# Performance work log

Hardware: AMD Instinct MI355X
Metric: run time of the kernel (lower is better)

## Reference

```python
import jax, jax.numpy as jnp
import numpy as np

NUM_HEADS = 16
INPUT_DIM = 1024  # == dim == qkv_scale


def setup_inputs() -> dict:
    key = jax.random.key(0)
    k1, k2, k3 = jax.random.split(key, 3)
    x = jax.random.normal(k1, (4, 2048, INPUT_DIM), dtype=jnp.float32)
    # torch Linear(input_dim, 3*dim): y = x @ W.T + b; we store W pre-transposed as [in, out]
    W_qkv = jax.random.normal(k2, (INPUT_DIM, 3 * INPUT_DIM), dtype=jnp.float32) * (INPUT_DIM ** -0.5)
    b_qkv = jax.random.normal(k3, (3 * INPUT_DIM,), dtype=jnp.float32) * 0.01
    return {"x": x, "W_qkv": W_qkv, "b_qkv": b_qkv}


def reference(x, W_qkv, b_qkv):
    b, n, _ = x.shape
    h = NUM_HEADS
    d = INPUT_DIM // h
    scale = INPUT_DIM ** 0.5  # qkv_scale**0.5, MULTIPLIED (no softmax, no division)

    qkv = x @ W_qkv + b_qkv                      # [b, n, 3*dim]
    # rearrange 'b n (h d k) -> k b h n d': last axis splits (h, d, 3), k fastest
    qkv = qkv.reshape(b, n, h, d, 3)
    q = jnp.transpose(qkv[..., 0], (0, 2, 1, 3))  # [b, h, n, d]
    k_ = jnp.transpose(qkv[..., 1], (0, 2, 1, 3))
    v = jnp.transpose(qkv[..., 2], (0, 2, 1, 3))

    attn = jnp.einsum('bhid,bhjd->bhij', q, k_) * scale  # [b, h, n, n]
    out = jnp.einsum('bhij,bhjd->bhid', attn, v)         # [b, h, n, d]
    return out
```

## Files before the change

kernel.cpp:

```cpp
#include <hip/hip_runtime.h>
#include <stdint.h>

#define DEV __device__ __forceinline__

typedef float f32x4 __attribute__((ext_vector_type(4)));
typedef __bf16 bf16x8 __attribute__((ext_vector_type(8)));
typedef short short8 __attribute__((ext_vector_type(8)));
typedef short short4v __attribute__((ext_vector_type(4)));

DEV unsigned short f2bf(float f) {
    union { float f; unsigned u; } c; c.f = f;
    unsigned u = c.u;
    u += 0x7fffu + ((u >> 16) & 1u);
    return (unsigned short)(u >> 16);
}

DEV void async_ld16(const void* g, void* l) {
    __builtin_amdgcn_global_load_lds(
        (const __attribute__((address_space(1))) unsigned int*)g,
        (__attribute__((address_space(3))) unsigned int*)l, 16, 0, 0);
}

DEV f32x4 mfma16(bf16x8 a, bf16x8 b, f32x4 c) {
    return __builtin_amdgcn_mfma_f32_16x16x32_bf16(a, b, c, 0, 0, 0);
}

__global__ __launch_bounds__(256) void k_prep(const float* __restrict__ x,
                                              const float* __restrict__ W,
                                              unsigned short* __restrict__ xb,
                                              unsigned short* __restrict__ Wt) {
    __shared__ float T[64][65];
    int blk = blockIdx.x;
    if (blk < 4096) {
        int t = blk * 256 + threadIdx.x;
        const float4* xp = (const float4*)x;
        float4 a = xp[t * 2], b = xp[t * 2 + 1];
        short8 o;
        o[0] = (short)f2bf(a.x); o[1] = (short)f2bf(a.y);
        o[2] = (short)f2bf(a.z); o[3] = (short)f2bf(a.w);
        o[4] = (short)f2bf(b.x); o[5] = (short)f2bf(b.y);
        o[6] = (short)f2bf(b.z); o[7] = (short)f2bf(b.w);
        *(short8*)(xb + t * 8) = o;
    } else {
        int bx = blk - 4096;
        int n0 = (bx % 48) * 64, k0 = (bx / 48) * 64;
        int t = threadIdx.x;
        int r = t >> 4, c4 = (t & 15) * 4;
        for (int i = 0; i < 4; i++) {
            int row = r + i * 16;
            float4 v = *(const float4*)(W + (k0 + row) * 3072 + n0 + c4);
            T[row][c4] = v.x; T[row][c4 + 1] = v.y; T[row][c4 + 2] = v.z; T[row][c4 + 3] = v.w;
        }
        __syncthreads();
        for (int i = 0; i < 4; i++) {
            int nrow = r + i * 16;
            short4v o;
            o[0] = (short)f2bf(T[c4 + 0][nrow]);
            o[1] = (short)f2bf(T[c4 + 1][nrow]);
            o[2] = (short)f2bf(T[c4 + 2][nrow]);
            o[3] = (short)f2bf(T[c4 + 3][nrow]);
            *(short4v*)(Wt + (n0 + nrow) * 1024 + k0 + c4) = o;
        }
    }
}

__global__ __launch_bounds__(256, 2) void k_qkv(const unsigned short* __restrict__ xb,
                                                const unsigned short* __restrict__ Wt,
                                                const float* __restrict__ bias,
                                                unsigned short* __restrict__ Q,
                                                unsigned short* __restrict__ K,
                                                unsigned short* __restrict__ V) {
    __shared__ __align__(16) unsigned short As[128 * 64];
    __shared__ __align__(16) unsigned short Bs[128 * 64];
    const int m0 = blockIdx.y * 128, n0 = blockIdx.x * 128;
    const int wave = threadIdx.x >> 6, lane = threadIdx.x & 63;
    const int wm = (wave & 1) * 64, wn = (wave >> 1) * 64;
    f32x4 acc[4][4] = {};
    const int slr = wave * 32 + (lane >> 3);
    const int scs = lane & 7;

    for (int kt = 0; kt < 16; kt++) {
        __syncthreads();
        for (int i = 0; i < 4; i++) {
            int lr = slr + i * 8;
            int c = scs ^ (lr & 7);
            async_ld16(xb + (m0 + lr) * 1024 + kt * 64 + c * 8,
                       (void*)(As + (wave * 32 + i * 8) * 64));
            async_ld16(Wt + (n0 + lr) * 1024 + kt * 64 + c * 8,
                       (void*)(Bs + (wave * 32 + i * 8) * 64));
        }
        __syncthreads();
        for (int ks = 0; ks < 2; ks++) {
            bf16x8 af[4], bfr[4];
            int c0 = ks * 4 + (lane >> 4);
            for (int tm = 0; tm < 4; tm++) {
                int row = wm + tm * 16 + (lane & 15);
                af[tm] = *(const bf16x8*)(As + row * 64 + (c0 ^ (row & 7)) * 8);
            }
            for (int tn = 0; tn < 4; tn++) {
                int row = wn + tn * 16 + (lane & 15);
                bfr[tn] = *(const bf16x8*)(Bs + row * 64 + (c0 ^ (row & 7)) * 8);
            }
            for (int tm = 0; tm < 4; tm++)
                for (int tn = 0; tn < 4; tn++)
                    acc[tm][tn] = mfma16(af[tm], bfr[tn], acc[tm][tn]);
        }
    }

    const int batch = m0 >> 11;
    for (int tn = 0; tn < 4; tn++) {
        int col = n0 + wn + tn * 16 + (lane & 15);
        int h = col / 192;
        int rem = col - h * 192;
        int d = rem / 3;
        int which = rem - d * 3;
        float bv = bias[col];
        int bh = batch * 16 + h;
        unsigned q_base = (unsigned)bh * 131072u + (unsigned)d;
        unsigned kv_base = ((unsigned)bh * 64u + (unsigned)d) * 2048u;
        unsigned short* dst = which == 0 ? Q : (which == 1 ? K : V);
        for (int tm = 0; tm < 4; tm++) {
            int rbase = m0 + wm + tm * 16 + ((lane >> 4) * 4);
            unsigned token0 = (unsigned)(rbase & 2047);
            float v0 = acc[tm][tn][0] + bv;
            float v1 = acc[tm][tn][1] + bv;
            float v2 = acc[tm][tn][2] + bv;
            float v3 = acc[tm][tn][3] + bv;
            if (which == 0) {
                unsigned idx = q_base + token0 * 64u;
                dst[idx]        = f2bf(v0 * 32.0f);
                dst[idx + 64u]  = f2bf(v1 * 32.0f);
                dst[idx + 128u] = f2bf(v2 * 32.0f);
                dst[idx + 192u] = f2bf(v3 * 32.0f);
            } else {
                uint2 p;
                p.x = (unsigned)f2bf(v0) | ((unsigned)f2bf(v1) << 16);
                p.y = (unsigned)f2bf(v2) | ((unsigned)f2bf(v3) << 16);
                *(uint2*)(dst + kv_base + token0) = p;
            }
        }
    }
}

__global__ __launch_bounds__(256) void k_attn3(const unsigned short* __restrict__ Kt,
                                               const unsigned short* __restrict__ Vt,
                                               const unsigned short* __restrict__ Q,
                                               float* __restrict__ out) {
    __shared__ __align__(16) float Ps[4][4096];
    __shared__ __align__(16) unsigned short Msb[4096];
    const int bh = blockIdx.x & 63, sub = blockIdx.x >> 6;
    const int wave = threadIdx.x >> 6, lane = threadIdx.x & 63;
    const int lan15 = lane & 15, quad = lane >> 4;
    const unsigned base = (unsigned)bh * 131072u;

    f32x4 acc[4][4] = {};
    for (int it = 0; it < 16; it++) {
        int no = wave * 512 + it * 32 + quad * 8;
        bf16x8 af[4], bfr[4];
        for (int mt = 0; mt < 4; mt++)
            af[mt] = *(const bf16x8*)(Kt + base + (unsigned)(mt * 16 + lan15) * 2048u + no);
        for (int nt = 0; nt < 4; nt++)
            bfr[nt] = *(const bf16x8*)(Vt + base + (unsigned)(nt * 16 + lan15) * 2048u + no);
        for (int mt = 0; mt < 4; mt++)
            for (int nt = 0; nt < 4; nt++)
                acc[mt][nt] = mfma16(af[mt], bfr[nt], acc[mt][nt]);
    }
    for (int mt = 0; mt < 4; mt++)
        for (int nt = 0; nt < 4; nt++)
            *(f32x4*)(&Ps[wave][((mt * 4 + nt) * 64 + lane) * 4]) = acc[mt][nt];
    __syncthreads();

    {
        int e0 = threadIdx.x * 16;
        for (int j = 0; j < 4; j++) {
            f32x4 m = *(const f32x4*)(&Ps[0][e0 + j * 4]);
            for (int s = 1; s < 4; s++) {
                f32x4 p = *(const f32x4*)(&Ps[s][e0 + j * 4]);
                m.x += p.x; m.y += p.y; m.z += p.z; m.w += p.w;
            }
            for (int r = 0; r < 4; r++) {
                int e = e0 + j * 4 + r;
                int tile = e >> 8, le = (e >> 2) & 63;
                int d1 = (tile >> 2) * 16 + ((le >> 4) << 2) + r;
                int d2 = (tile & 3) * 16 + (le & 15);
                Msb[d2 * 64 + (((d1 >> 3) ^ (d2 & 7)) << 3) + (d1 & 7)] = f2bf(m[r]);
            }
        }
    }
    __syncthreads();

    {
        const int q0w = sub * 256 + wave * 64;
        f32x4 oacc[4][4] = {};
#pragma unroll
        for (int ks = 0; ks < 2; ks++) {
            bf16x8 af[4], bfr[4];
            for (int mt = 0; mt < 4; mt++)
                af[mt] = *(const bf16x8*)(Q + base + (unsigned)(q0w + mt * 16 + lan15) * 64u +
                                          ks * 32 + quad * 8);
            for (int nt = 0; nt < 4; nt++) {
                int d2 = nt * 16 + lan15;
                bfr[nt] = *(const bf16x8*)(Msb + d2 * 64 + (((ks * 4 + quad) ^ (d2 & 7)) << 3));
            }
            for (int mt = 0; mt < 4; mt++)
                for (int nt = 0; nt < 4; nt++)
                    oacc[mt][nt] = mfma16(af[mt], bfr[nt], oacc[mt][nt]);
        }
        for (int mt = 0; mt < 4; mt++)
            for (int nt = 0; nt < 4; nt++)
                for (int r = 0; r < 4; r++)
                    out[base + (unsigned)(q0w + mt * 16 + quad * 4 + r) * 64u + nt * 16 + lan15] =
                        oacc[mt][nt][r];
    }
}

extern "C" void kernel_launch(void* const* d_in, const int* in_sizes, int n_in,
                              void* d_out, int out_size, void* d_ws, size_t ws_size,
                              hipStream_t stream) {
    const float* x = (const float*)d_in[0];
    const float* W = (const float*)d_in[1];
    const float* b = (const float*)d_in[2];
    float* out = (float*)d_out;

    unsigned short* xb = (unsigned short*)d_ws;
    unsigned short* Wt = xb + 8388608;
    unsigned short* Qb = Wt + 3145728;
    unsigned short* Kt = Qb + 8388608;
    unsigned short* Vt = Kt + 8388608;

    k_prep<<<4864, 256, 0, stream>>>(x, W, xb, Wt);
    k_qkv<<<dim3(24, 64), 256, 0, stream>>>(xb, Wt, b, Qb, Kt, Vt);
    k_attn3<<<512, 256, 0, stream>>>(Kt, Vt, Qb, out);
}
```

Before: 184.9 us.

## Reassociate K^T V through the input Gram matrix and drop K/V materialization

Instead of computing K and V for all tokens, the attention core K^T V is rewritten as Wk^T (X^T X) Wv plus bias correction terms that use per-batch column sums of x. New kernels compute the per-batch Gram matrix X^T X (syrk-style, full not symmetric), multiply it by Wv, contract with Wk per head, and add the bias terms. Q alone is projected, and a final small GEMM applies Q to the per-head 64x64 matrix. This cuts projection FLOPs and removes the large K/V intermediates. In exchange it adds a transposed copy of x, more kernel launches, and bf16 rounding of large Gram entries, which may cost accuracy.

```diff
diff --git a/kernel.cpp b/kernel.cpp
--- a/kernel.cpp
+++ b/kernel.cpp
@@ -14,13 +14,14 @@
     u += 0x7fffu + ((u >> 16) & 1u);
     return (unsigned short)(u >> 16);
 }
-
+DEV float bf2f(unsigned short u) {
+    union { unsigned u; float f; } c; c.u = ((unsigned)u) << 16; return c.f;
+}
 DEV void async_ld16(const void* g, void* l) {
     __builtin_amdgcn_global_load_lds(
         (const __attribute__((address_space(1))) unsigned int*)g,
         (__attribute__((address_space(3))) unsigned int*)l, 16, 0, 0);
 }
-
 DEV f32x4 mfma16(bf16x8 a, bf16x8 b, f32x4 c) {
     return __builtin_amdgcn_mfma_f32_16x16x32_bf16(a, b, c, 0, 0, 0);
 }
@@ -28,53 +29,84 @@
 __global__ __launch_bounds__(256) void k_prep(const float* __restrict__ x,
                                               const float* __restrict__ W,
                                               unsigned short* __restrict__ xb,
-                                              unsigned short* __restrict__ Wt) {
+                                              unsigned short* __restrict__ xt,
+                                              unsigned short* __restrict__ Wt,
+                                              float* __restrict__ s) {
     __shared__ float T[64][65];
-    int blk = blockIdx.x;
-    if (blk < 4096) {
-        int t = blk * 256 + threadIdx.x;
-        const float4* xp = (const float4*)x;
-        float4 a = xp[t * 2], b = xp[t * 2 + 1];
-        short8 o;
-        o[0] = (short)f2bf(a.x); o[1] = (short)f2bf(a.y);
-        o[2] = (short)f2bf(a.z); o[3] = (short)f2bf(a.w);
-        o[4] = (short)f2bf(b.x); o[5] = (short)f2bf(b.y);
-        o[6] = (short)f2bf(b.z); o[7] = (short)f2bf(b.w);
-        *(short8*)(xb + t * 8) = o;
-    } else {
-        int bx = blk - 4096;
-        int n0 = (bx % 48) * 64, k0 = (bx / 48) * 64;
-        int t = threadIdx.x;
-        int r = t >> 4, c4 = (t & 15) * 4;
-        for (int i = 0; i < 4; i++) {
-            int row = r + i * 16;
-            float4 v = *(const float4*)(W + (k0 + row) * 3072 + n0 + c4);
+    const int blk = blockIdx.x, t = threadIdx.x;
+    if (blk < 2048) {
+        int batch = blk >> 9, r512 = blk & 511;
+        int t0 = (r512 >> 4) * 64, d0 = (r512 & 15) * 64;
+        int rr = t >> 4, c4 = (t & 15) * 4;
+        for (int i = 0; i < 4; i++) {
+            int row = rr + i * 16;
+            float4 v = *(const float4*)(x + (unsigned)(batch * 2048 + t0 + row) * 1024u + d0 + c4);
             T[row][c4] = v.x; T[row][c4 + 1] = v.y; T[row][c4 + 2] = v.z; T[row][c4 + 3] = v.w;
-        }
-        __syncthreads();
-        for (int i = 0; i < 4; i++) {
-            int nrow = r + i * 16;
+            short4v o;
+            o[0] = (short)f2bf(v.x); o[1] = (short)f2bf(v.y);
+            o[2] = (short)f2bf(v.z); o[3] = (short)f2bf(v.w);
+            *(short4v*)(xb + (unsigned)(batch * 2048 + t0 + row) * 1024u + d0 + c4) = o;
+        }
+        __syncthreads();
+        for (int i = 0; i < 4; i++) {
+            int nrow = rr + i * 16;
             short4v o;
             o[0] = (short)f2bf(T[c4 + 0][nrow]);
             o[1] = (short)f2bf(T[c4 + 1][nrow]);
             o[2] = (short)f2bf(T[c4 + 2][nrow]);
             o[3] = (short)f2bf(T[c4 + 3][nrow]);
-            *(short4v*)(Wt + (n0 + nrow) * 1024 + k0 + c4) = o;
-        }
-    }
-}
-
-__global__ __launch_bounds__(256, 2) void k_qkv(const unsigned short* __restrict__ xb,
-                                                const unsigned short* __restrict__ Wt,
-                                                const float* __restrict__ bias,
-                                                unsigned short* __restrict__ Q,
-                                                unsigned short* __restrict__ K,
-                                                unsigned short* __restrict__ V) {
+            *(short4v*)(xt + (unsigned)(batch * 1024 + d0 + nrow) * 2048u + t0 + c4) = o;
+        }
+    } else if (blk < 2816) {
+        int bx = blk - 2048;
+        int k0 = (bx / 48) * 64, n0 = (bx % 48) * 64;
+        int rr = t >> 4, c4 = (t & 15) * 4;
+        for (int i = 0; i < 4; i++) {
+            int row = rr + i * 16;
+            float4 v = *(const float4*)(W + (unsigned)(k0 + row) * 3072u + n0 + c4);
+            T[row][c4] = v.x; T[row][c4 + 1] = v.y; T[row][c4 + 2] = v.z; T[row][c4 + 3] = v.w;
+        }
+        __syncthreads();
+        for (int i = 0; i < 4; i++) {
+            int ncol = rr + i * 16;
+            int n = n0 + ncol;
+            int which = n % 3;
+            int oc = (n / 192) * 64 + (n % 192) / 3;
+            short4v o;
+            o[0] = (short)f2bf(T[c4 + 0][ncol]);
+            o[1] = (short)f2bf(T[c4 + 1][ncol]);
+            o[2] = (short)f2bf(T[c4 + 2][ncol]);
+            o[3] = (short)f2bf(T[c4 + 3][ncol]);
+            *(short4v*)(Wt + (unsigned)which * 1048576u + (unsigned)oc * 1024u + k0 + c4) = o;
+        }
+    } else {
+        int idx = blk - 2816;
+        int batch = idx >> 4, dg = idx & 15;
+        int col = dg * 64 + (t & 63), rg = t >> 6;
+        float a = 0.0f;
+        for (int r = rg * 512; r < rg * 512 + 512; r++)
+            a += x[(unsigned)(batch * 2048 + r) * 1024u + col];
+        ((float*)T)[rg * 64 + (t & 63)] = a;
+        __syncthreads();
+        if (t < 64) {
+            float v = ((float*)T)[t] + ((float*)T)[64 + t] +
+                      ((float*)T)[128 + t] + ((float*)T)[192 + t];
+            s[batch * 1024 + dg * 64 + t] = v;
+        }
+    }
+}
+
+__global__ __launch_bounds__(256, 2) void k_q(const unsigned short* __restrict__ Wt,
+                                              const unsigned short* __restrict__ xb,
+                                              const float* __restrict__ bias,
+                                              unsigned short* __restrict__ Qs) {
     __shared__ __align__(16) unsigned short As[128 * 64];
     __shared__ __align__(16) unsigned short Bs[128 * 64];
-    const int m0 = blockIdx.y * 128, n0 = blockIdx.x * 128;
+    const int m0 = blockIdx.x * 128;
+    const int n0 = blockIdx.y * 128;
     const int wave = threadIdx.x >> 6, lane = threadIdx.x & 63;
     const int wm = (wave & 1) * 64, wn = (wave >> 1) * 64;
+    const int lan15 = lane & 15, quad = lane >> 4;
     f32x4 acc[4][4] = {};
     const int slr = wave * 32 + (lane >> 3);
     const int scs = lane & 7;
@@ -84,21 +116,21 @@
         for (int i = 0; i < 4; i++) {
             int lr = slr + i * 8;
             int c = scs ^ (lr & 7);
-            async_ld16(xb + (m0 + lr) * 1024 + kt * 64 + c * 8,
+            async_ld16(Wt + (unsigned)(m0 + lr) * 1024u + kt * 64 + c * 8,
                        (void*)(As + (wave * 32 + i * 8) * 64));
-            async_ld16(Wt + (n0 + lr) * 1024 + kt * 64 + c * 8,
+            async_ld16(xb + (unsigned)(n0 + lr) * 1024u + kt * 64 + c * 8,
                        (void*)(Bs + (wave * 32 + i * 8) * 64));
         }
         __syncthreads();
         for (int ks = 0; ks < 2; ks++) {
             bf16x8 af[4], bfr[4];
-            int c0 = ks * 4 + (lane >> 4);
+            int c0 = ks * 4 + quad;
             for (int tm = 0; tm < 4; tm++) {
-                int row = wm + tm * 16 + (lane & 15);
+                int row = wm + tm * 16 + lan15;
                 af[tm] = *(const bf16x8*)(As + row * 64 + (c0 ^ (row & 7)) * 8);
             }
             for (int tn = 0; tn < 4; tn++) {
-                int row = wn + tn * 16 + (lane & 15);
+                int row = wn + tn * 16 + lan15;
                 bfr[tn] = *(const bf16x8*)(Bs + row * 64 + (c0 ^ (row & 7)) * 8);
             }
             for (int tm = 0; tm < 4; tm++)
@@ -107,111 +139,245 @@
         }
     }
 
-    const int batch = m0 >> 11;
-    for (int tn = 0; tn < 4; tn++) {
-        int col = n0 + wn + tn * 16 + (lane & 15);
-        int h = col / 192;
-        int rem = col - h * 192;
-        int d = rem / 3;
-        int which = rem - d * 3;
-        float bv = bias[col];
-        int bh = batch * 16 + h;
-        unsigned q_base = (unsigned)bh * 131072u + (unsigned)d;
-        unsigned kv_base = ((unsigned)bh * 64u + (unsigned)d) * 2048u;
-        unsigned short* dst = which == 0 ? Q : (which == 1 ? K : V);
-        for (int tm = 0; tm < 4; tm++) {
-            int rbase = m0 + wm + tm * 16 + ((lane >> 4) * 4);
-            unsigned token0 = (unsigned)(rbase & 2047);
-            float v0 = acc[tm][tn][0] + bv;
-            float v1 = acc[tm][tn][1] + bv;
-            float v2 = acc[tm][tn][2] + bv;
-            float v3 = acc[tm][tn][3] + bv;
-            if (which == 0) {
-                unsigned idx = q_base + token0 * 64u;
-                dst[idx]        = f2bf(v0 * 32.0f);
-                dst[idx + 64u]  = f2bf(v1 * 32.0f);
-                dst[idx + 128u] = f2bf(v2 * 32.0f);
-                dst[idx + 192u] = f2bf(v3 * 32.0f);
-            } else {
-                uint2 p;
-                p.x = (unsigned)f2bf(v0) | ((unsigned)f2bf(v1) << 16);
-                p.y = (unsigned)f2bf(v2) | ((unsigned)f2bf(v3) << 16);
-                *(uint2*)(dst + kv_base + token0) = p;
-            }
-        }
-    }
-}
-
-__global__ __launch_bounds__(256) void k_attn3(const unsigned short* __restrict__ Kt,
-                                               const unsigned short* __restrict__ Vt,
-                                               const unsigned short* __restrict__ Q,
-                                               float* __restrict__ out) {
-    __shared__ __align__(16) float Ps[4][4096];
-    __shared__ __align__(16) unsigned short Msb[4096];
-    const int bh = blockIdx.x & 63, sub = blockIdx.x >> 6;
+    for (int tm = 0; tm < 4; tm++) {
+        int oc = m0 + wm + tm * 16 + quad * 4;
+        int h = oc >> 6, dd = oc & 63;
+        float b0 = bias[h * 192 + (dd + 0) * 3];
+        float b1 = bias[h * 192 + (dd + 1) * 3];
+        float b2 = bias[h * 192 + (dd + 2) * 3];
+        float b3 = bias[h * 192 + (dd + 3) * 3];
+        for (int tn = 0; tn < 4; tn++) {
+            int token = n0 + wn + tn * 16 + lan15;
+            unsigned bb = (unsigned)(token >> 11), tl = (unsigned)(token & 2047);
+            uint2 p;
+            p.x = (unsigned)f2bf((acc[tm][tn][0] + b0) * 32.0f) |
+                  ((unsigned)f2bf((acc[tm][tn][1] + b1) * 32.0f) << 16);
+            p.y = (unsigned)f2bf((acc[tm][tn][2] + b2) * 32.0f) |
+                  ((unsigned)f2bf((acc[tm][tn][3] + b3) * 32.0f) << 16);
+            *(uint2*)(Qs + bb * 2097152u + tl * 1024u + oc) = p;
+        }
+    }
+}
+
+__global__ __launch_bounds__(256, 2) void k_syrk(const unsigned short* __restrict__ xt,
+                                                 unsigned short* __restrict__ G) {
+    __shared__ __align__(16) unsigned short As[64 * 64];
+    __shared__ __align__(16) unsigned short Bs[128 * 64];
+    const int b = blockIdx.z;
+    const int i0 = blockIdx.x * 64, j0 = blockIdx.y * 128;
+    const int wave = threadIdx.x >> 6, lane = threadIdx.x & 63;
+    const int wm = (wave & 1) * 32, wn = (wave >> 1) * 64;
+    const int lan15 = lane & 15, quad = lane >> 4;
+    const unsigned xbase = (unsigned)b * 2097152u;
+    f32x4 acc[2][4] = {};
+    const int slrA = wave * 16 + (lane >> 3);
+    const int slrB = wave * 32 + (lane >> 3);
+    const int scs = lane & 7;
+
+    for (int kt = 0; kt < 32; kt++) {
+        __syncthreads();
+        for (int i = 0; i < 2; i++) {
+            int lr = slrA + i * 8;
+            int c = scs ^ (lr & 7);
+            async_ld16(xt + xbase + (unsigned)(i0 + lr) * 2048u + kt * 64 + c * 8,
+                       (void*)(As + (wave * 16 + i * 8) * 64));
+        }
+        for (int i = 0; i < 4; i++) {
+            int lr = slrB + i * 8;
+            int c = scs ^ (lr & 7);
+            async_ld16(xt + xbase + (unsigned)(j0 + lr) * 2048u + kt * 64 + c * 8,
+                       (void*)(Bs + (wave * 32 + i * 8) * 64));
+        }
+        __syncthreads();
+        for (int ks = 0; ks < 2; ks++) {
+            bf16x8 af[2], bfr[4];
+            int c0 = ks * 4 + quad;
+            for (int tm = 0; tm < 2; tm++) {
+                int row = wm + tm * 16 + lan15;
+                af[tm] = *(const bf16x8*)(As + row * 64 + (c0 ^ (row & 7)) * 8);
+            }
+            for (int tn = 0; tn < 4; tn++) {
+                int row = wn + tn * 16 + lan15;
+                bfr[tn] = *(const bf16x8*)(Bs + row * 64 + (c0 ^ (row & 7)) * 8);
+            }
+            for (int tm = 0; tm < 2; tm++)
+                for (int tn = 0; tn < 4; tn++)
+                    acc[tm][tn] = mfma16(af[tm], bfr[tn], acc[tm][tn]);
+        }
+    }
+    const unsigned gbase = (unsigned)b * 1048576u;
+    for (int tm = 0; tm < 2; tm++) {
+        int d1q = i0 + wm + tm * 16 + quad * 4;
+        for (int tn = 0; tn < 4; tn++) {
+            int d2 = j0 + wn + tn * 16 + lan15;
+            uint2 p;
+            p.x = (unsigned)f2bf(acc[tm][tn][0]) | ((unsigned)f2bf(acc[tm][tn][1]) << 16);
+            p.y = (unsigned)f2bf(acc[tm][tn][2]) | ((unsigned)f2bf(acc[tm][tn][3]) << 16);
+            *(uint2*)(G + gbase + (unsigned)d2 * 1024u + d1q) = p;
+        }
+    }
+}
+
+__global__ __launch_bounds__(256, 2) void k_gv(const unsigned short* __restrict__ G,
+                                               const unsigned short* __restrict__ Wt,
+                                               unsigned short* __restrict__ GVt) {
+    __shared__ __align__(16) unsigned short As[64 * 64];
+    __shared__ __align__(16) unsigned short Bs[128 * 64];
+    const int b = blockIdx.z;
+    const int i0 = blockIdx.x * 64;
+    const int j0 = blockIdx.y * 128;
+    const int wave = threadIdx.x >> 6, lane = threadIdx.x & 63;
+    const int wm = (wave & 1) * 32, wn = (wave >> 1) * 64;
+    const int lan15 = lane & 15, quad = lane >> 4;
+    const unsigned gbase = (unsigned)b * 1048576u;
+    const unsigned short* Wv = Wt + 2097152u;
+    f32x4 acc[2][4] = {};
+    const int slrA = wave * 16 + (lane >> 3);
+    const int slrB = wave * 32 + (lane >> 3);
+    const int scs = lane & 7;
+
+    for (int kt = 0; kt < 16; kt++) {
+        __syncthreads();
+        for (int i = 0; i < 2; i++) {
+            int lr = slrA + i * 8;
+            int c = scs ^ (lr & 7);
+            async_ld16(G + gbase + (unsigned)(i0 + lr) * 1024u + kt * 64 + c * 8,
+                       (void*)(As + (wave * 16 + i * 8) * 64));
+        }
+        for (int i = 0; i < 4; i++) {
+            int lr = slrB + i * 8;
+            int c = scs ^ (lr & 7);
+            async_ld16(Wv + (unsigned)(j0 + lr) * 1024u + kt * 64 + c * 8,
+                       (void*)(Bs + (wave * 32 + i * 8) * 64));
+        }
+        __syncthreads();
+        for (int ks = 0; ks < 2; ks++) {
+            bf16x8 af[2], bfr[4];
+            int c0 = ks * 4 + quad;
+            for (int tm = 0; tm < 2; tm++) {
+                int row = wm + tm * 16 + lan15;
+                af[tm] = *(const bf16x8*)(As + row * 64 + (c0 ^ (row & 7)) * 8);
+            }
+            for (int tn = 0; tn < 4; tn++) {
+                int row = wn + tn * 16 + lan15;
+                bfr[tn] = *(const bf16x8*)(Bs + row * 64 + (c0 ^ (row & 7)) * 8);
+            }
+            for (int tm = 0; tm < 2; tm++)
+                for (int tn = 0; tn < 4; tn++)
+                    acc[tm][tn] = mfma16(af[tm], bfr[tn], acc[tm][tn]);
+        }
+    }
+    for (int tm = 0; tm < 2; tm++) {
+        int rq = i0 + wm + tm * 16 + quad * 4;
+        for (int tn = 0; tn < 4; tn++) {
+            int vcol = j0 + wn + tn * 16 + lan15;
+            uint2 p;
+            p.x = (unsigned)f2bf(acc[tm][tn][0]) | ((unsigned)f2bf(acc[tm][tn][1]) << 16);
+            p.y = (unsigned)f2bf(acc[tm][tn][2]) | ((unsigned)f2bf(acc[tm][tn][3]) << 16);
+            *(uint2*)(GVt + gbase + (unsigned)vcol * 1024u + rq) = p;
+        }
+    }
+}
+
+__global__ __launch_bounds__(256) void k_mp(const unsigned short* __restrict__ Wt,
+                                            const unsigned short* __restrict__ GVt,
+                                            const float* __restrict__ s,
+                                            const float* __restrict__ bias,
+                                            unsigned short* __restrict__ Mt) {
+    __shared__ __align__(16) float Ss[3 * 4096 + 128];
+    const int bh = blockIdx.x, b = bh >> 4, h = bh & 15;
     const int wave = threadIdx.x >> 6, lane = threadIdx.x & 63;
     const int lan15 = lane & 15, quad = lane >> 4;
-    const unsigned base = (unsigned)bh * 131072u;
-
+    const unsigned short* Wk = Wt + 1048576u + (unsigned)(h * 64) * 1024u;
+    const unsigned short* GVh = GVt + (unsigned)b * 1048576u + (unsigned)(h * 64) * 1024u;
     f32x4 acc[4][4] = {};
-    for (int it = 0; it < 16; it++) {
-        int no = wave * 512 + it * 32 + quad * 8;
+    for (int it = 0; it < 8; it++) {
+        int ko = wave * 256 + it * 32 + quad * 8;
         bf16x8 af[4], bfr[4];
         for (int mt = 0; mt < 4; mt++)
-            af[mt] = *(const bf16x8*)(Kt + base + (unsigned)(mt * 16 + lan15) * 2048u + no);
+            af[mt] = *(const bf16x8*)(Wk + (unsigned)(mt * 16 + lan15) * 1024u + ko);
         for (int nt = 0; nt < 4; nt++)
-            bfr[nt] = *(const bf16x8*)(Vt + base + (unsigned)(nt * 16 + lan15) * 2048u + no);
+            bfr[nt] = *(const bf16x8*)(GVh + (unsigned)(nt * 16 + lan15) * 1024u + ko);
         for (int mt = 0; mt < 4; mt++)
             for (int nt = 0; nt < 4; nt++)
                 acc[mt][nt] = mfma16(af[mt], bfr[nt], acc[mt][nt]);
     }
+    if (wave >= 1)
+        for (int mt = 0; mt < 4; mt++)
+            for (int nt = 0; nt < 4; nt++)
+                *(f32x4*)(&Ss[(wave - 1) * 4096 + ((mt * 4 + nt) * 64 + lane) * 4]) = acc[mt][nt];
+
+    float* t1 = Ss + 12288;
+    float* t2 = t1 + 64;
+    const int tt = threadIdx.x;
+    if (tt < 128) {
+        int d = tt & 63;
+        const unsigned short* wrow = Wt + (tt < 64 ? 1048576u : 2097152u) +
+                                     (unsigned)(h * 64 + d) * 1024u;
+        const float* sb = s + b * 1024;
+        float a = 0.0f;
+        for (int r = 0; r < 1024; r += 8) {
+            short8 w8 = *(const short8*)(wrow + r);
+            for (int j = 0; j < 8; j++)
+                a += bf2f((unsigned short)w8[j]) * sb[r + j];
+        }
+        (tt < 64 ? t1 : t2)[d] = a;
+    }
+    __syncthreads();
+    if (wave == 0) {
+        for (int mt = 0; mt < 4; mt++)
+            for (int nt = 0; nt < 4; nt++) {
+                f32x4 m = acc[mt][nt];
+                for (int w = 0; w < 3; w++) {
+                    f32x4 p = *(const f32x4*)(&Ss[w * 4096 + ((mt * 4 + nt) * 64 + lane) * 4]);
+                    m.x += p.x; m.y += p.y; m.z += p.z; m.w += p.w;
+                }
+                int d2 = nt * 16 + lan15;
+                float bv = bias[h * 192 + d2 * 3 + 2];
+                float tw = t2[d2];
+                unsigned short v[4];
+                for (int r = 0; r < 4; r++) {
+                    int d1 = mt * 16 + quad * 4 + r;
+                    float bk = bias[h * 192 + d1 * 3 + 1];
+                    v[r] = f2bf(m[r] + t1[d1] * bv + bk * tw + 2048.0f * bk * bv);
+                }
+                uint2 p;
+                p.x = (unsigned)v[0] | ((unsigned)v[1] << 16);
+                p.y = (unsigned)v[2] | ((unsigned)v[3] << 16);
+                *(uint2*)(Mt + (unsigned)bh * 4096u + (unsigned)d2 * 64u +
+                          mt * 16 + quad * 4) = p;
+            }
+    }
+}
+
+__global__ __launch_bounds__(256) void k_out(const unsigned short* __restrict__ Qs,
+                                             const unsigned short* __restrict__ Mt,
+                                             float* __restrict__ out) {
+    const int bh = blockIdx.y, b = bh >> 4, h = bh & 15;
+    const int wave = threadIdx.x >> 6, lane = threadIdx.x & 63;
+    const int lan15 = lane & 15, quad = lane >> 4;
+    const int t0w = blockIdx.x * 256 + wave * 64;
+    f32x4 acc[4][4] = {};
+#pragma unroll
+    for (int ks = 0; ks < 2; ks++) {
+        bf16x8 af[4], bfr[4];
+        for (int mt = 0; mt < 4; mt++) {
+            int tok = t0w + mt * 16 + lan15;
+            af[mt] = *(const bf16x8*)(Qs + (unsigned)b * 2097152u + (unsigned)tok * 1024u +
+                                      h * 64 + ks * 32 + quad * 8);
+        }
+        for (int nt = 0; nt < 4; nt++)
+            bfr[nt] = *(const bf16x8*)(Mt + (unsigned)bh * 4096u +
+                                       (unsigned)(nt * 16 + lan15) * 64u + ks * 32 + quad * 8);
+        for (int mt = 0; mt < 4; mt++)
+            for (int nt = 0; nt < 4; nt++)
+                acc[mt][nt] = mfma16(af[mt], bfr[nt], acc[mt][nt]);
+    }
     for (int mt = 0; mt < 4; mt++)
         for (int nt = 0; nt < 4; nt++)
-            *(f32x4*)(&Ps[wave][((mt * 4 + nt) * 64 + lane) * 4]) = acc[mt][nt];
-    __syncthreads();
-
-    {
-        int e0 = threadIdx.x * 16;
-        for (int j = 0; j < 4; j++) {
-            f32x4 m = *(const f32x4*)(&Ps[0][e0 + j * 4]);
-            for (int s = 1; s < 4; s++) {
-                f32x4 p = *(const f32x4*)(&Ps[s][e0 + j * 4]);
-                m.x += p.x; m.y += p.y; m.z += p.z; m.w += p.w;
-            }
-            for (int r = 0; r < 4; r++) {
-                int e = e0 + j * 4 + r;
-                int tile = e >> 8, le = (e >> 2) & 63;
-                int d1 = (tile >> 2) * 16 + ((le >> 4) << 2) + r;
-                int d2 = (tile & 3) * 16 + (le & 15);
-                Msb[d2 * 64 + (((d1 >> 3) ^ (d2 & 7)) << 3) + (d1 & 7)] = f2bf(m[r]);
-            }
-        }
-    }
-    __syncthreads();
-
-    {
-        const int q0w = sub * 256 + wave * 64;
-        f32x4 oacc[4][4] = {};
-#pragma unroll
-        for (int ks = 0; ks < 2; ks++) {
-            bf16x8 af[4], bfr[4];
-            for (int mt = 0; mt < 4; mt++)
-                af[mt] = *(const bf16x8*)(Q + base + (unsigned)(q0w + mt * 16 + lan15) * 64u +
-                                          ks * 32 + quad * 8);
-            for (int nt = 0; nt < 4; nt++) {
-                int d2 = nt * 16 + lan15;
-                bfr[nt] = *(const bf16x8*)(Msb + d2 * 64 + (((ks * 4 + quad) ^ (d2 & 7)) << 3));
-            }
-            for (int mt = 0; mt < 4; mt++)
-                for (int nt = 0; nt < 4; nt++)
-                    oacc[mt][nt] = mfma16(af[mt], bfr[nt], oacc[mt][nt]);
-        }
-        for (int mt = 0; mt < 4; mt++)
-            for (int nt = 0; nt < 4; nt++)
-                for (int r = 0; r < 4; r++)
-                    out[base + (unsigned)(q0w + mt * 16 + quad * 4 + r) * 64u + nt * 16 + lan15] =
-                        oacc[mt][nt][r];
-    }
+            for (int r = 0; r < 4; r++)
+                out[(unsigned)bh * 131072u + (unsigned)(t0w + mt * 16 + quad * 4 + r) * 64u +
+                    nt * 16 + lan15] = acc[mt][nt][r];
 }
 
 extern "C" void kernel_launch(void* const* d_in, const int* in_sizes, int n_in,
@@ -223,12 +389,18 @@
     float* out = (float*)d_out;
 
     unsigned short* xb = (unsigned short*)d_ws;
-    unsigned short* Wt = xb + 8388608;
-    unsigned short* Qb = Wt + 3145728;
-    unsigned short* Kt = Qb + 8388608;
-    unsigned short* Vt = Kt + 8388608;
-
-    k_prep<<<4864, 256, 0, stream>>>(x, W, xb, Wt);
-    k_qkv<<<dim3(24, 64), 256, 0, stream>>>(xb, Wt, b, Qb, Kt, Vt);
-    k_attn3<<<512, 256, 0, stream>>>(Kt, Vt, Qb, out);
-}
+    unsigned short* xt = xb + 8388608;
+    unsigned short* Wt = xt + 8388608;
+    unsigned short* Qs = Wt + 3145728;
+    unsigned short* G  = Qs + 8388608;
+    unsigned short* Mt = G + 4194304;
+    float* s = (float*)(Mt + 262144);
+    unsigned short* GVt = xt;
+
+    k_prep<<<2880, 256, 0, stream>>>(x, W, xb, xt, Wt, s);
+    k_q<<<dim3(8, 64), 256, 0, stream>>>(Wt, xb, b, Qs);
+    k_syrk<<<dim3(16, 8, 4), 256, 0, stream>>>(xt, G);
+    k_gv<<<dim3(16, 8, 4), 256, 0, stream>>>(G, Wt, GVt);
+    k_mp<<<64, 256, 0, stream>>>(Wt, GVt, s, b, Mt);
+    k_out<<<dim3(8, 64), 256, 0, stream>>>(Qs, Mt, out);
+}
```

New measurement: 337.1 us. +82.3%, slower.

## Split QKV projection into Q and KV GEMMs with plane-separated weights

Applied to the files above, without the earlier changes.

The weight transpose now reorders columns into separate Q, K and V planes. The single QKV GEMM is split into a Q kernel, computed transposed so its output is written as packed 8-byte stores in a token-major layout, and a KV kernel that writes K and V transposed. This removes the scattered 2-byte Q stores. The attention kernel now stages K and V tiles into LDS with async loads and splits the 64x64 K^T V product across waves by output tile, which drops the fp32 per-wave partial reduction through LDS. The cost is an extra kernel launch, and each block still recomputes the full K^T V product.

```diff
diff --git a/kernel.cpp b/kernel.cpp
--- a/kernel.cpp
+++ b/kernel.cpp
@@ -14,13 +14,11 @@
     u += 0x7fffu + ((u >> 16) & 1u);
     return (unsigned short)(u >> 16);
 }
-
 DEV void async_ld16(const void* g, void* l) {
     __builtin_amdgcn_global_load_lds(
         (const __attribute__((address_space(1))) unsigned int*)g,
         (__attribute__((address_space(3))) unsigned int*)l, 16, 0, 0);
 }
-
 DEV f32x4 mfma16(bf16x8 a, bf16x8 b, f32x4 c) {
     return __builtin_amdgcn_mfma_f32_16x16x32_bf16(a, b, c, 0, 0, 0);
 }
@@ -30,51 +28,53 @@
                                               unsigned short* __restrict__ xb,
                                               unsigned short* __restrict__ Wt) {
     __shared__ float T[64][65];
-    int blk = blockIdx.x;
+    const int blk = blockIdx.x, t = threadIdx.x;
     if (blk < 4096) {
-        int t = blk * 256 + threadIdx.x;
+        int i = blk * 256 + t;
         const float4* xp = (const float4*)x;
-        float4 a = xp[t * 2], b = xp[t * 2 + 1];
+        float4 a = xp[i * 2], b = xp[i * 2 + 1];
         short8 o;
         o[0] = (short)f2bf(a.x); o[1] = (short)f2bf(a.y);
         o[2] = (short)f2bf(a.z); o[3] = (short)f2bf(a.w);
         o[4] = (short)f2bf(b.x); o[5] = (short)f2bf(b.y);
         o[6] = (short)f2bf(b.z); o[7] = (short)f2bf(b.w);
-        *(short8*)(xb + t * 8) = o;
+        *(short8*)(xb + i * 8) = o;
     } else {
         int bx = blk - 4096;
-        int n0 = (bx % 48) * 64, k0 = (bx / 48) * 64;
-        int t = threadIdx.x;
-        int r = t >> 4, c4 = (t & 15) * 4;
-        for (int i = 0; i < 4; i++) {
-            int row = r + i * 16;
-            float4 v = *(const float4*)(W + (k0 + row) * 3072 + n0 + c4);
+        int k0 = (bx / 48) * 64, n0 = (bx % 48) * 64;
+        int rr = t >> 4, c4 = (t & 15) * 4;
+        for (int i = 0; i < 4; i++) {
+            int row = rr + i * 16;
+            float4 v = *(const float4*)(W + (unsigned)(k0 + row) * 3072u + n0 + c4);
             T[row][c4] = v.x; T[row][c4 + 1] = v.y; T[row][c4 + 2] = v.z; T[row][c4 + 3] = v.w;
         }
         __syncthreads();
         for (int i = 0; i < 4; i++) {
-            int nrow = r + i * 16;
+            int ncol = rr + i * 16;
+            int n = n0 + ncol;
+            int which = n % 3;
+            int oc = (n / 192) * 64 + (n % 192) / 3;
             short4v o;
-            o[0] = (short)f2bf(T[c4 + 0][nrow]);
-            o[1] = (short)f2bf(T[c4 + 1][nrow]);
-            o[2] = (short)f2bf(T[c4 + 2][nrow]);
-            o[3] = (short)f2bf(T[c4 + 3][nrow]);
-            *(short4v*)(Wt + (n0 + nrow) * 1024 + k0 + c4) = o;
-        }
-    }
-}
-
-__global__ __launch_bounds__(256, 2) void k_qkv(const unsigned short* __restrict__ xb,
-                                                const unsigned short* __restrict__ Wt,
-                                                const float* __restrict__ bias,
-                                                unsigned short* __restrict__ Q,
-                                                unsigned short* __restrict__ K,
-                                                unsigned short* __restrict__ V) {
+            o[0] = (short)f2bf(T[c4 + 0][ncol]);
+            o[1] = (short)f2bf(T[c4 + 1][ncol]);
+            o[2] = (short)f2bf(T[c4 + 2][ncol]);
+            o[3] = (short)f2bf(T[c4 + 3][ncol]);
+            *(short4v*)(Wt + (unsigned)which * 1048576u + (unsigned)oc * 1024u + k0 + c4) = o;
+        }
+    }
+}
+
+__global__ __launch_bounds__(256, 2) void k_q(const unsigned short* __restrict__ Wt,
+                                              const unsigned short* __restrict__ xb,
+                                              const float* __restrict__ bias,
+                                              unsigned short* __restrict__ Qs) {
     __shared__ __align__(16) unsigned short As[128 * 64];
     __shared__ __align__(16) unsigned short Bs[128 * 64];
-    const int m0 = blockIdx.y * 128, n0 = blockIdx.x * 128;
+    const int m0 = blockIdx.x * 128;
+    const int n0 = blockIdx.y * 128;
     const int wave = threadIdx.x >> 6, lane = threadIdx.x & 63;
     const int wm = (wave & 1) * 64, wn = (wave >> 1) * 64;
+    const int lan15 = lane & 15, quad = lane >> 4;
     f32x4 acc[4][4] = {};
     const int slr = wave * 32 + (lane >> 3);
     const int scs = lane & 7;
@@ -84,21 +84,21 @@
         for (int i = 0; i < 4; i++) {
             int lr = slr + i * 8;
             int c = scs ^ (lr & 7);
-            async_ld16(xb + (m0 + lr) * 1024 + kt * 64 + c * 8,
+            async_ld16(Wt + (unsigned)(m0 + lr) * 1024u + kt * 64 + c * 8,
                        (void*)(As + (wave * 32 + i * 8) * 64));
-            async_ld16(Wt + (n0 + lr) * 1024 + kt * 64 + c * 8,
+            async_ld16(xb + (unsigned)(n0 + lr) * 1024u + kt * 64 + c * 8,
                        (void*)(Bs + (wave * 32 + i * 8) * 64));
         }
         __syncthreads();
         for (int ks = 0; ks < 2; ks++) {
             bf16x8 af[4], bfr[4];
-            int c0 = ks * 4 + (lane >> 4);
+            int c0 = ks * 4 + quad;
             for (int tm = 0; tm < 4; tm++) {
-                int row = wm + tm * 16 + (lane & 15);
+                int row = wm + tm * 16 + lan15;
                 af[tm] = *(const bf16x8*)(As + row * 64 + (c0 ^ (row & 7)) * 8);
             }
             for (int tn = 0; tn < 4; tn++) {
-                int row = wn + tn * 16 + (lane & 15);
+                int row = wn + tn * 16 + lan15;
                 bfr[tn] = *(const bf16x8*)(Bs + row * 64 + (c0 ^ (row & 7)) * 8);
             }
             for (int tm = 0; tm < 4; tm++)
@@ -107,111 +107,175 @@
         }
     }
 
+    for (int tm = 0; tm < 4; tm++) {
+        int oc = m0 + wm + tm * 16 + quad * 4;
+        int h = oc >> 6, dd = oc & 63;
+        float b0 = bias[h * 192 + (dd + 0) * 3];
+        float b1 = bias[h * 192 + (dd + 1) * 3];
+        float b2 = bias[h * 192 + (dd + 2) * 3];
+        float b3 = bias[h * 192 + (dd + 3) * 3];
+        for (int tn = 0; tn < 4; tn++) {
+            int token = n0 + wn + tn * 16 + lan15;
+            unsigned bb = (unsigned)(token >> 11), tl = (unsigned)(token & 2047);
+            uint2 p;
+            p.x = (unsigned)f2bf((acc[tm][tn][0] + b0) * 32.0f) |
+                  ((unsigned)f2bf((acc[tm][tn][1] + b1) * 32.0f) << 16);
+            p.y = (unsigned)f2bf((acc[tm][tn][2] + b2) * 32.0f) |
+                  ((unsigned)f2bf((acc[tm][tn][3] + b3) * 32.0f) << 16);
+            *(uint2*)(Qs + bb * 2097152u + tl * 1024u + oc) = p;
+        }
+    }
+}
+
+__global__ __launch_bounds__(256, 2) void k_kv(const unsigned short* __restrict__ xb,
+                                               const unsigned short* __restrict__ Wt,
+                                               const float* __restrict__ bias,
+                                               unsigned short* __restrict__ K,
+                                               unsigned short* __restrict__ V) {
+    __shared__ __align__(16) unsigned short As[128 * 64];
+    __shared__ __align__(16) unsigned short Bs[128 * 64];
+    const int m0 = blockIdx.y * 128;
+    const int n0 = blockIdx.x * 128;
+    const int plane = 1 + (n0 >> 10);
+    const int pc0 = n0 & 1023;
+    const unsigned short* Wp = Wt + (unsigned)plane * 1048576u;
+    const int wave = threadIdx.x >> 6, lane = threadIdx.x & 63;
+    const int wm = (wave & 1) * 64, wn = (wave >> 1) * 64;
+    const int lan15 = lane & 15, quad = lane >> 4;
+    f32x4 acc[4][4] = {};
+    const int slr = wave * 32 + (lane >> 3);
+    const int scs = lane & 7;
+
+    for (int kt = 0; kt < 16; kt++) {
+        __syncthreads();
+        for (int i = 0; i < 4; i++) {
+            int lr = slr + i * 8;
+            int c = scs ^ (lr & 7);
+            async_ld16(xb + (unsigned)(m0 + lr) * 1024u + kt * 64 + c * 8,
+                       (void*)(As + (wave * 32 + i * 8) * 64));
+            async_ld16(Wp + (unsigned)(pc0 + lr) * 1024u + kt * 64 + c * 8,
+                       (void*)(Bs + (wave * 32 + i * 8) * 64));
+        }
+        __syncthreads();
+        for (int ks = 0; ks < 2; ks++) {
+            bf16x8 af[4], bfr[4];
+            int c0 = ks * 4 + quad;
+            for (int tm = 0; tm < 4; tm++) {
+                int row = wm + tm * 16 + lan15;
+                af[tm] = *(const bf16x8*)(As + row * 64 + (c0 ^ (row & 7)) * 8);
+            }
+            for (int tn = 0; tn < 4; tn++) {
+                int row = wn + tn * 16 + lan15;
+                bfr[tn] = *(const bf16x8*)(Bs + row * 64 + (c0 ^ (row & 7)) * 8);
+            }
+            for (int tm = 0; tm < 4; tm++)
+                for (int tn = 0; tn < 4; tn++)
+                    acc[tm][tn] = mfma16(af[tm], bfr[tn], acc[tm][tn]);
+        }
+    }
+
     const int batch = m0 >> 11;
+    unsigned short* dst = (plane == 1) ? K : V;
     for (int tn = 0; tn < 4; tn++) {
-        int col = n0 + wn + tn * 16 + (lane & 15);
-        int h = col / 192;
-        int rem = col - h * 192;
-        int d = rem / 3;
-        int which = rem - d * 3;
-        float bv = bias[col];
-        int bh = batch * 16 + h;
-        unsigned q_base = (unsigned)bh * 131072u + (unsigned)d;
-        unsigned kv_base = ((unsigned)bh * 64u + (unsigned)d) * 2048u;
-        unsigned short* dst = which == 0 ? Q : (which == 1 ? K : V);
+        int cip = pc0 + wn + tn * 16 + lan15;
+        int h = cip >> 6, d = cip & 63;
+        float bv = bias[h * 192 + d * 3 + plane];
+        unsigned kv_base = ((unsigned)(batch * 16 + h) * 64u + (unsigned)d) * 2048u;
         for (int tm = 0; tm < 4; tm++) {
-            int rbase = m0 + wm + tm * 16 + ((lane >> 4) * 4);
+            int rbase = m0 + wm + tm * 16 + quad * 4;
             unsigned token0 = (unsigned)(rbase & 2047);
-            float v0 = acc[tm][tn][0] + bv;
-            float v1 = acc[tm][tn][1] + bv;
-            float v2 = acc[tm][tn][2] + bv;
-            float v3 = acc[tm][tn][3] + bv;
-            if (which == 0) {
-                unsigned idx = q_base + token0 * 64u;
-                dst[idx]        = f2bf(v0 * 32.0f);
-                dst[idx + 64u]  = f2bf(v1 * 32.0f);
-                dst[idx + 128u] = f2bf(v2 * 32.0f);
-                dst[idx + 192u] = f2bf(v3 * 32.0f);
-            } else {
-                uint2 p;
-                p.x = (unsigned)f2bf(v0) | ((unsigned)f2bf(v1) << 16);
-                p.y = (unsigned)f2bf(v2) | ((unsigned)f2bf(v3) << 16);
-                *(uint2*)(dst + kv_base + token0) = p;
-            }
-        }
-    }
-}
-
-__global__ __launch_bounds__(256) void k_attn3(const unsigned short* __restrict__ Kt,
+            uint2 p;
+            p.x = (unsigned)f2bf(acc[tm][tn][0] + bv) |
+                  ((unsigned)f2bf(acc[tm][tn][1] + bv) << 16);
+            p.y = (unsigned)f2bf(acc[tm][tn][2] + bv) |
+                  ((unsigned)f2bf(acc[tm][tn][3] + bv) << 16);
+            *(uint2*)(dst + kv_base + token0) = p;
+        }
+    }
+}
+
+__global__ __launch_bounds__(256) void k_attn4(const unsigned short* __restrict__ Kt,
                                                const unsigned short* __restrict__ Vt,
-                                               const unsigned short* __restrict__ Q,
+                                               const unsigned short* __restrict__ Qs,
                                                float* __restrict__ out) {
-    __shared__ __align__(16) float Ps[4][4096];
-    __shared__ __align__(16) unsigned short Msb[4096];
+    __shared__ __align__(16) unsigned short Ks[64 * 128];
+    __shared__ __align__(16) unsigned short Vs[64 * 128];
+    __shared__ __align__(16) unsigned short Msb[64 * 64];
     const int bh = blockIdx.x & 63, sub = blockIdx.x >> 6;
+    const int b = bh >> 4, h = bh & 15;
     const int wave = threadIdx.x >> 6, lane = threadIdx.x & 63;
     const int lan15 = lane & 15, quad = lane >> 4;
     const unsigned base = (unsigned)bh * 131072u;
-
-    f32x4 acc[4][4] = {};
-    for (int it = 0; it < 16; it++) {
-        int no = wave * 512 + it * 32 + quad * 8;
+    const int mt0 = (wave & 1) * 2, nt0 = (wave >> 1) * 2;
+    const int slr = wave * 16 + (lane >> 4), scs = lane & 15;
+
+    f32x4 macc[2][2] = {};
+    for (int j = 0; j < 16; j++) {
+        __syncthreads();
+        for (int i = 0; i < 4; i++) {
+            int lr = slr + i * 4;
+            int c = scs ^ (lr & 15);
+            async_ld16(Kt + base + (unsigned)lr * 2048u + j * 128 + c * 8,
+                       (void*)(Ks + (wave * 16 + i * 4) * 128));
+            async_ld16(Vt + base + (unsigned)lr * 2048u + j * 128 + c * 8,
+                       (void*)(Vs + (wave * 16 + i * 4) * 128));
+        }
+        __syncthreads();
+        for (int ks2 = 0; ks2 < 4; ks2++) {
+            int c0 = ks2 * 4 + quad;
+            bf16x8 ak[2], bv[2];
+            for (int i = 0; i < 2; i++) {
+                int row = (mt0 + i) * 16 + lan15;
+                ak[i] = *(const bf16x8*)(Ks + row * 128 + (c0 ^ (row & 15)) * 8);
+            }
+            for (int i = 0; i < 2; i++) {
+                int row = (nt0 + i) * 16 + lan15;
+                bv[i] = *(const bf16x8*)(Vs + row * 128 + (c0 ^ (row & 15)) * 8);
+            }
+            for (int i = 0; i < 2; i++)
+                for (int j2 = 0; j2 < 2; j2++)
+                    macc[i][j2] = mfma16(ak[i], bv[j2], macc[i][j2]);
+        }
+    }
+    for (int i = 0; i < 2; i++)
+        for (int j2 = 0; j2 < 2; j2++) {
+            int d2 = (nt0 + j2) * 16 + lan15;
+            int c4 = ((mt0 + i) * 4 + quad) ^ (d2 & 15);
+            uint2 p;
+            p.x = (unsigned)f2bf(macc[i][j2][0]) | ((unsigned)f2bf(macc[i][j2][1]) << 16);
+            p.y = (unsigned)f2bf(macc[i][j2][2]) | ((unsigned)f2bf(macc[i][j2][3]) << 16);
+            *(uint2*)(Msb + d2 * 64 + c4 * 4) = p;
+        }
+    __syncthreads();
+
+    const int t0 = sub * 256 + wave * 64;
+    f32x4 oacc[4][4] = {};
+#pragma unroll
+    for (int ks = 0; ks < 2; ks++) {
         bf16x8 af[4], bfr[4];
-        for (int mt = 0; mt < 4; mt++)
-            af[mt] = *(const bf16x8*)(Kt + base + (unsigned)(mt * 16 + lan15) * 2048u + no);
-        for (int nt = 0; nt < 4; nt++)
-            bfr[nt] = *(const bf16x8*)(Vt + base + (unsigned)(nt * 16 + lan15) * 2048u + no);
+        for (int mt = 0; mt < 4; mt++) {
+            int tok = t0 + mt * 16 + lan15;
+            af[mt] = *(const bf16x8*)(Qs + (unsigned)b * 2097152u + (unsigned)tok * 1024u +
+                                      h * 64 + ks * 32 + quad * 8);
+        }
+        for (int nt = 0; nt < 4; nt++) {
+            int d2 = nt * 16 + lan15;
+            int cA = ks * 8 + quad * 2;
+            uint2 u0 = *(const uint2*)(Msb + d2 * 64 + ((cA) ^ (d2 & 15)) * 4);
+            uint2 u1 = *(const uint2*)(Msb + d2 * 64 + ((cA + 1) ^ (d2 & 15)) * 4);
+            union { uint4 u; bf16x8 v; } cv;
+            cv.u.x = u0.x; cv.u.y = u0.y; cv.u.z = u1.x; cv.u.w = u1.y;
+            bfr[nt] = cv.v;
+        }
         for (int mt = 0; mt < 4; mt++)
             for (int nt = 0; nt < 4; nt++)
-                acc[mt][nt] = mfma16(af[mt], bfr[nt], acc[mt][nt]);
+                oacc[mt][nt] = mfma16(af[mt], bfr[nt], oacc[mt][nt]);
     }
     for (int mt = 0; mt < 4; mt++)
         for (int nt = 0; nt < 4; nt++)
-            *(f32x4*)(&Ps[wave][((mt * 4 + nt) * 64 + lane) * 4]) = acc[mt][nt];
-    __syncthreads();
-
-    {
-        int e0 = threadIdx.x * 16;
-        for (int j = 0; j < 4; j++) {
-            f32x4 m = *(const f32x4*)(&Ps[0][e0 + j * 4]);
-            for (int s = 1; s < 4; s++) {
-                f32x4 p = *(const f32x4*)(&Ps[s][e0 + j * 4]);
-                m.x += p.x; m.y += p.y; m.z += p.z; m.w += p.w;
-            }
-            for (int r = 0; r < 4; r++) {
-                int e = e0 + j * 4 + r;
-                int tile = e >> 8, le = (e >> 2) & 63;
-                int d1 = (tile >> 2) * 16 + ((le >> 4) << 2) + r;
-                int d2 = (tile & 3) * 16 + (le & 15);
-                Msb[d2 * 64 + (((d1 >> 3) ^ (d2 & 7)) << 3) + (d1 & 7)] = f2bf(m[r]);
-            }
-        }
-    }
-    __syncthreads();
-
-    {
-        const int q0w = sub * 256 + wave * 64;
-        f32x4 oacc[4][4] = {};
-#pragma unroll
-        for (int ks = 0; ks < 2; ks++) {
-            bf16x8 af[4], bfr[4];
-            for (int mt = 0; mt < 4; mt++)
-                af[mt] = *(const bf16x8*)(Q + base + (unsigned)(q0w + mt * 16 + lan15) * 64u +
-                                          ks * 32 + quad * 8);
-            for (int nt = 0; nt < 4; nt++) {
-                int d2 = nt * 16 + lan15;
-                bfr[nt] = *(const bf16x8*)(Msb + d2 * 64 + (((ks * 4 + quad) ^ (d2 & 7)) << 3));
-            }
-            for (int mt = 0; mt < 4; mt++)
-                for (int nt = 0; nt < 4; nt++)
-                    oacc[mt][nt] = mfma16(af[mt], bfr[nt], oacc[mt][nt]);
-        }
-        for (int mt = 0; mt < 4; mt++)
-            for (int nt = 0; nt < 4; nt++)
-                for (int r = 0; r < 4; r++)
-                    out[base + (unsigned)(q0w + mt * 16 + quad * 4 + r) * 64u + nt * 16 + lan15] =
-                        oacc[mt][nt][r];
-    }
+            for (int r = 0; r < 4; r++)
+                out[base + (unsigned)(t0 + mt * 16 + quad * 4 + r) * 64u + nt * 16 + lan15] =
+                    oacc[mt][nt][r];
 }
 
 extern "C" void kernel_launch(void* const* d_in, const int* in_sizes, int n_in,
@@ -224,11 +288,12 @@
 
     unsigned short* xb = (unsigned short*)d_ws;
     unsigned short* Wt = xb + 8388608;
-    unsigned short* Qb = Wt + 3145728;
-    unsigned short* Kt = Qb + 8388608;
+    unsigned short* Qs = Wt + 3145728;
+    unsigned short* Kt = Qs + 8388608;
     unsigned short* Vt = Kt + 8388608;
 
     k_prep<<<4864, 256, 0, stream>>>(x, W, xb, Wt);
-    k_qkv<<<dim3(24, 64), 256, 0, stream>>>(xb, Wt, b, Qb, Kt, Vt);
-    k_attn3<<<512, 256, 0, stream>>>(Kt, Vt, Qb, out);
-}
+    k_q<<<dim3(8, 64), 256, 0, stream>>>(Wt, xb, b, Qs);
+    k_kv<<<dim3(16, 64), 256, 0, stream>>>(xb, Wt, b, Kt, Vt);
+    k_attn4<<<512, 256, 0, stream>>>(Kt, Vt, Qs, out);
+}
```

After: 182.6 us. About the same (-1.2%).
